# Kernel optimization log

Hardware: AMD Instinct MI355X
Metric: run time of the kernel (lower is better)

Reference implementation:

```python
import jax, jax.numpy as jnp
import numpy as np

N_NODES = 50000
N_EDGES = 640000
IN_F, H1, H2, H3, N_CLS = 128, 128, 128, 128, 40


def setup_inputs() -> dict:
    key = jax.random.key(0)
    ks = jax.random.split(key, 16)
    def lin(k, i, o):
        bound = 1.0 / np.sqrt(i)
        kw, kb = jax.random.split(k)
        W = jax.random.uniform(kw, (i, o), jnp.float32, -bound, bound)
        b = jax.random.uniform(kb, (o,), jnp.float32, -bound, bound)
        return W, b
    Wr, br = lin(ks[0], IN_F, H3)
    W1, b1 = lin(ks[1], IN_F, H1)
    W2, b2 = lin(ks[2], H1, H2)
    W3, b3 = lin(ks[3], H2, H3)
    Wop, bop = lin(ks[4], H3, N_CLS)
    x = jax.random.normal(ks[5], (N_NODES, IN_F), jnp.float32)
    src = jax.random.randint(ks[6], (N_EDGES,), 0, N_NODES, jnp.int64)
    dst = jax.random.randint(ks[7], (N_EDGES,), 0, N_NODES, jnp.int64)
    edge_weight = jax.random.uniform(ks[8], (N_EDGES,), jnp.float32)
    return {"x": x, "src": src, "dst": dst, "edge_weight": edge_weight,
            "Wr": Wr, "br": br, "W1": W1, "b1": b1, "W2": W2, "b2": b2,
            "W3": W3, "b3": b3, "Wop": Wop, "bop": bop}


def _gconv(x, src, dst, ew, W, b, n_nodes):
    # gather neighbor features, scale by edge weight, scatter-sum to dst, linear
    msg = x[src] * ew[:, None]                      # [E, d_in]
    agg = jax.ops.segment_sum(msg, dst, num_segments=n_nodes)  # [N, d_in]
    return agg @ W + b


def reference(x, src, dst, edge_weight, Wr, br, W1, b1, W2, b2, W3, b3, Wop, bop):
    n = x.shape[0]
    res = x @ Wr + br
    h = jax.nn.relu(_gconv(x, src, dst, edge_weight, W1, b1, n))
    h = jax.nn.relu(_gconv(h, src, dst, edge_weight, W2, b2, n))
    h = _gconv(h, src, dst, edge_weight, W3, b3, n)
    h = jax.nn.relu(h + res)
    return h @ Wop + bop
```

## Files before the change

kernel.cpp:

```cpp
#include <hip/hip_runtime.h>
#include <hip/hip_fp16.h>
#include <stdint.h>


#define NF 128

typedef unsigned short u16;
typedef unsigned int u32;
typedef __attribute__((ext_vector_type(8))) short short8;
typedef __attribute__((ext_vector_type(4))) float f32x4;

__device__ __forceinline__ float bf2f(u16 v) {
    union { unsigned u; float f; } x; x.u = (unsigned)v << 16; return x.f;
}
__device__ __forceinline__ u16 f2bf(float f) {
    union { float f; unsigned u; } x; x.f = f;
    unsigned r = (x.u + 0x7FFFu + ((x.u >> 16) & 1u)) >> 16;
    return (u16)r;
}

__global__ __launch_bounds__(256) void prep_all(
    const int* __restrict__ dst, int* __restrict__ counts, int* __restrict__ rank,
    int n_edges,
    const float* __restrict__ x, u16* __restrict__ xb, int n_feat,
    const float* __restrict__ Wr, const float* __restrict__ W1,
    const float* __restrict__ W2, const float* __restrict__ W3,
    const float* __restrict__ Wop, u16* __restrict__ Wt, u16* __restrict__ Wtop,
    int HB, int CB)
{
    int b = blockIdx.x;
    if (b < HB) {
        int e = b * 256 + threadIdx.x;
        if (e < n_edges) rank[e] = atomicAdd(&counts[dst[e]], 1);
    } else if (b < HB + CB) {
        int idx = ((b - HB) * 256 + threadIdx.x) * 4;
        if (idx < n_feat) {
            float4 v = *reinterpret_cast<const float4*>(x + idx);
            ushort4 o;
            o.x = f2bf(v.x); o.y = f2bf(v.y); o.z = f2bf(v.z); o.w = f2bf(v.w);
            *reinterpret_cast<ushort4*>(xb + idx) = o;
        }
    } else {
        int i = (b - HB - CB) * 256 + threadIdx.x;
        if (i < 4 * 16384) {
            int w = i >> 14, r = i & 16383;
            int nn = r >> 7, kk = r & 127;
            const float* W = (w == 0) ? Wr : (w == 1) ? W1 : (w == 2) ? W2 : W3;
            Wt[i] = f2bf(W[kk * NF + nn]);
        } else {
            int r = i - 4 * 16384;
            if (r < 48 * 128) {
                int nn = r >> 7, kk = r & 127;
                Wtop[r] = (nn < 40) ? f2bf(Wop[kk * 40 + nn]) : (u16)0;
            }
        }
    }
}

__global__ __launch_bounds__(256) void scan_pass1(
    const int* __restrict__ counts, int* __restrict__ bsums, int n)
{
    __shared__ int s[256];
    int i = blockIdx.x * 256 + threadIdx.x;
    int c = (i < n) ? counts[i] : 0;
    s[threadIdx.x] = (c + 3) & ~3;
    __syncthreads();
    for (int off = 128; off > 0; off >>= 1) {
        if (threadIdx.x < off) s[threadIdx.x] += s[threadIdx.x + off];
        __syncthreads();
    }
    if (threadIdx.x == 0) bsums[blockIdx.x] = s[0];
}

__global__ __launch_bounds__(256) void scan_pass23(
    int* __restrict__ rowptr, const int* __restrict__ bsums,
    u32* __restrict__ ppairs, int n, int G)
{
    __shared__ int s[256];
    int t = threadIdx.x;
    int bv = (t < G) ? bsums[t] : 0;
    s[t] = bv;
    __syncthreads();
    for (int off = 1; off < 256; off <<= 1) {
        int u = (t >= off) ? s[t - off] : 0;
        __syncthreads();
        s[t] += u;
        __syncthreads();
    }
    int blockoff = (blockIdx.x > 0) ? s[blockIdx.x - 1] : 0;
    int total = s[255];
    __syncthreads();

    int i = blockIdx.x * 256 + t;
    int c = (i < n) ? rowptr[i] : 0;
    int v = (c + 3) & ~3;
    s[t] = v;
    __syncthreads();
    for (int off = 1; off < 256; off <<= 1) {
        int u = (t >= off) ? s[t - off] : 0;
        __syncthreads();
        s[t] += u;
        __syncthreads();
    }
    int excl = s[t] - v + blockoff;
    if (i < n) {
        rowptr[i] = excl;
        for (int k = c; k < v; ++k) ppairs[excl + k] = 0u;
    }
    if (i == 0) rowptr[n] = total;
}

__global__ __launch_bounds__(256) void fill_res(
    const int* __restrict__ src, const int* __restrict__ dst,
    const float* __restrict__ ew, const int* __restrict__ rowptr,
    const int* __restrict__ rank, u32* __restrict__ ppairs, int n_edges,
    const u16* __restrict__ A, const u16* __restrict__ Wt,
    const float* __restrict__ bias, u16* __restrict__ resout, int nrows,
    int HB)
{
    __shared__ u16 Bs[128 * 128];
    if (blockIdx.x < (u32)HB) {
        int e = blockIdx.x * 256 + threadIdx.x;
        if (e >= n_edges) return;
        int pos = rowptr[dst[e]] + rank[e];
        ppairs[pos] = ((u32)src[e] << 16) |
                      (u32)__half_as_ushort(__float2half_rn(ew[e]));
        return;
    }
    const int bid = blockIdx.x - HB;
    const int tid = threadIdx.x;
    #pragma unroll
    for (int i = 0; i < 8; i++) {
        int G = tid + i * 256;
        int row = G >> 4, g = G & 15, gs = g ^ (row & 7);
        *reinterpret_cast<short8*>(&Bs[row * NF + gs * 8]) =
            *reinterpret_cast<const short8*>(Wt + (size_t)G * 8);
    }

    const int wave = tid >> 6, lane = tid & 63;
    const int lrow = lane & 15, lk = lane >> 4;
    const int row0 = bid * 64 + wave * 16;
    const int grow = row0 + lrow;

    short8 a[4];
    if (grow < nrows) {
        const u16* Ar = A + (size_t)grow * NF + lk * 8;
        #pragma unroll
        for (int t = 0; t < 4; t++)
            a[t] = *reinterpret_cast<const short8*>(Ar + t * 32);
    } else {
        #pragma unroll
        for (int t = 0; t < 4; t++)
            #pragma unroll
            for (int j = 0; j < 8; j++) a[t][j] = 0;
    }
    __syncthreads();

    f32x4 acc[8];
    #pragma unroll
    for (int c = 0; c < 8; c++) { acc[c][0]=0.f; acc[c][1]=0.f; acc[c][2]=0.f; acc[c][3]=0.f; }

    #pragma unroll
    for (int t = 0; t < 4; t++) {
        #pragma unroll
        for (int c = 0; c < 8; c++) {
            int col = c * 16 + lrow;
            int g = t * 4 + lk, gs = g ^ (col & 7);
            short8 b = *reinterpret_cast<const short8*>(&Bs[col * NF + gs * 8]);
            acc[c] = __builtin_amdgcn_mfma_f32_16x16x32_bf16(a[t], b, acc[c], 0, 0, 0);
        }
    }

    #pragma unroll
    for (int c = 0; c < 8; c++) {
        int col = c * 16 + lrow;
        float bv = bias[col];
        #pragma unroll
        for (int r = 0; r < 4; r++) {
            int orow = row0 + lk * 4 + r;
            if (orow < nrows)
                resout[(size_t)orow * NF + col] = f2bf(acc[c][r] + bv);
        }
    }
}

template<int RES, int PROJ>
__global__ __launch_bounds__(256) void layer_gg(
    const u16* __restrict__ X, const int* __restrict__ rowptr,
    const u32* __restrict__ ppairs, const u16* __restrict__ Wt,
    const float* __restrict__ bias, const u16* __restrict__ resid,
    const u16* __restrict__ Wtop, const float* __restrict__ bop,
    u16* __restrict__ hout, float* __restrict__ out, int n_nodes)
{
    __shared__ u16 As[16 * 128];
    __shared__ u16 Hs[16 * 128];

    const int tid = threadIdx.x;
    const int node0 = blockIdx.x * 16;

    {
        const int nl = tid >> 4;
        const int fl = tid & 15;
        const int node = node0 + nl;
        float acc[8];
        #pragma unroll
        for (int j = 0; j < 8; j++) acc[j] = 0.f;

        if (node < n_nodes) {
            const u16* xf = X + fl * 8;
            int e0 = rowptr[node];
            int e1 = rowptr[node + 1];
            int e = e0;
            for (; e + 8 <= e1; e += 8) {
                uint4 pa = *reinterpret_cast<const uint4*>(ppairs + e);
                uint4 pb = *reinterpret_cast<const uint4*>(ppairs + e + 4);
                u32 p[8] = {pa.x, pa.y, pa.z, pa.w, pb.x, pb.y, pb.z, pb.w};
                short8 v[8];
                #pragma unroll
                for (int k = 0; k < 8; k++)
                    v[k] = *reinterpret_cast<const short8*>(xf + (size_t)(p[k] >> 16) * NF);
                #pragma unroll
                for (int k = 0; k < 8; k++) {
                    float w = __half2float(__ushort_as_half((u16)(p[k] & 0xFFFFu)));
                    #pragma unroll
                    for (int j = 0; j < 8; j++)
                        acc[j] = fmaf(bf2f((u16)v[k][j]), w, acc[j]);
                }
            }
            if (e < e1) {
                uint4 pa = *reinterpret_cast<const uint4*>(ppairs + e);
                u32 p[4] = {pa.x, pa.y, pa.z, pa.w};
                short8 v[4];
                #pragma unroll
                for (int k = 0; k < 4; k++)
                    v[k] = *reinterpret_cast<const short8*>(xf + (size_t)(p[k] >> 16) * NF);
                #pragma unroll
                for (int k = 0; k < 4; k++) {
                    float w = __half2float(__ushort_as_half((u16)(p[k] & 0xFFFFu)));
                    #pragma unroll
                    for (int j = 0; j < 8; j++)
                        acc[j] = fmaf(bf2f((u16)v[k][j]), w, acc[j]);
                }
            }
        }
        short8 o;
        #pragma unroll
        for (int j = 0; j < 8; j++) o[j] = (short)f2bf(acc[j]);
        int gs = fl ^ (nl & 7);
        *reinterpret_cast<short8*>(&As[nl * NF + gs * 8]) = o;
    }
    __syncthreads();

    const int wave = tid >> 6, lane = tid & 63;
    const int lrow = lane & 15, lk = lane >> 4;

    short8 a[4];
    #pragma unroll
    for (int t = 0; t < 4; t++) {
        int g = t * 4 + lk, gs = g ^ (lrow & 7);
        a[t] = *reinterpret_cast<const short8*>(&As[lrow * NF + gs * 8]);
    }

    f32x4 acc2[2];
    #pragma unroll
    for (int ct = 0; ct < 2; ct++) { acc2[ct][0]=0.f; acc2[ct][1]=0.f; acc2[ct][2]=0.f; acc2[ct][3]=0.f; }

    #pragma unroll
    for (int t = 0; t < 4; t++) {
        #pragma unroll
        for (int ct = 0; ct < 2; ct++) {
            int col = wave * 32 + ct * 16 + lrow;
            short8 b = *reinterpret_cast<const short8*>(Wt + (size_t)col * NF + (t * 4 + lk) * 8);
            acc2[ct] = __builtin_amdgcn_mfma_f32_16x16x32_bf16(a[t], b, acc2[ct], 0, 0, 0);
        }
    }

    #pragma unroll
    for (int ct = 0; ct < 2; ct++) {
        int col = wave * 32 + ct * 16 + lrow;
        float bv = bias[col];
        #pragma unroll
        for (int r = 0; r < 4; r++) {
            int row = lk * 4 + r;
            int node = node0 + row;
            if (node < n_nodes) {
                float v = acc2[ct][r] + bv;
                if (RES) v += bf2f(resid[(size_t)node * NF + col]);
                v = fmaxf(v, 0.f);
                if (!PROJ) {
                    hout[(size_t)node * NF + col] = f2bf(v);
                } else {
                    Hs[row * NF + (((col >> 3) ^ (row & 7)) << 3) + (col & 7)] = f2bf(v);
                }
            }
        }
    }

    if (PROJ) {
        __syncthreads();
        if (wave < 3) {
            short8 pa[4];
            #pragma unroll
            for (int t = 0; t < 4; t++) {
                int g = t * 4 + lk, gs = g ^ (lrow & 7);
                pa[t] = *reinterpret_cast<const short8*>(&Hs[lrow * NF + gs * 8]);
            }
            f32x4 pacc;
            pacc[0]=0.f; pacc[1]=0.f; pacc[2]=0.f; pacc[3]=0.f;
            int col = wave * 16 + lrow;
            #pragma unroll
            for (int t = 0; t < 4; t++) {
                short8 b = *reinterpret_cast<const short8*>(Wtop + (size_t)col * NF + (t * 4 + lk) * 8);
                pacc = __builtin_amdgcn_mfma_f32_16x16x32_bf16(pa[t], b, pacc, 0, 0, 0);
            }
            if (col < 40) {
                float bv = bop[col];
                #pragma unroll
                for (int r = 0; r < 4; r++) {
                    int node = node0 + lk * 4 + r;
                    if (node < n_nodes)
                        out[(size_t)node * 40 + col] = pacc[r] + bv;
                }
            }
        }
    }
}


extern "C" void kernel_launch(void* const* d_in, const int* in_sizes, int n_in,
                              void* d_out, int out_size, void* d_ws, size_t ws_size,
                              hipStream_t stream)
{
    const float* x   = (const float*)d_in[0];
    const int*   src = (const int*)d_in[1];
    const int*   dst = (const int*)d_in[2];
    const float* ew  = (const float*)d_in[3];
    const float* Wr  = (const float*)d_in[4];
    const float* br  = (const float*)d_in[5];
    const float* W1  = (const float*)d_in[6];
    const float* b1  = (const float*)d_in[7];
    const float* W2  = (const float*)d_in[8];
    const float* b2  = (const float*)d_in[9];
    const float* W3  = (const float*)d_in[10];
    const float* b3  = (const float*)d_in[11];
    const float* Wop = (const float*)d_in[12];
    const float* bop = (const float*)d_in[13];
    float* out = (float*)d_out;

    const int n_nodes = in_sizes[0] / NF;
    const int n_edges = in_sizes[1];
    const size_t feat = (size_t)n_nodes * NF;

    u16* xb   = (u16*)d_ws;
    u16* h1b  = xb + feat;
    u16* h2b  = h1b + feat;
    u16* resb = h2b + feat;
    u16* Wt   = resb + feat;
    u16* Wtop = Wt + 4 * 16384;
    int* rowptr = (int*)(Wtop + 48 * 128);
    const int G1 = (n_nodes + 255) / 256;
    int* bsums  = rowptr + (n_nodes + 1);
    int* rank   = bsums + (G1 + 1);
    u32* ppairs = (u32*)(((uintptr_t)(rank + n_edges) + 15) & ~(uintptr_t)15);

    const int HB = (n_edges + 255) / 256;
    const int CB = ((int)feat / 4 + 255) / 256;
    const int PB = (4 * 16384 + 48 * 128 + 255) / 256;
    const int RG = (n_nodes + 63) / 64;
    const int layer_grid = (n_nodes + 15) / 16;

    hipMemsetAsync(rowptr, 0, (size_t)(n_nodes + 1) * sizeof(int), stream);
    prep_all<<<HB + CB + PB, 256, 0, stream>>>(
        dst, rowptr, rank, n_edges, x, xb, (int)feat,
        Wr, W1, W2, W3, Wop, Wt, Wtop, HB, CB);
    scan_pass1<<<G1, 256, 0, stream>>>(rowptr, bsums, n_nodes);
    scan_pass23<<<G1, 256, 0, stream>>>(rowptr, bsums, ppairs, n_nodes, G1);

    fill_res<<<HB + RG, 256, 0, stream>>>(
        src, dst, ew, rowptr, rank, ppairs, n_edges,
        xb, Wt, br, resb, n_nodes, HB);

    layer_gg<0, 0><<<layer_grid, 256, 0, stream>>>(
        xb, rowptr, ppairs, Wt + 16384, b1, nullptr, nullptr, nullptr,
        h1b, nullptr, n_nodes);
    layer_gg<0, 0><<<layer_grid, 256, 0, stream>>>(
        h1b, rowptr, ppairs, Wt + 2 * 16384, b2, nullptr, nullptr, nullptr,
        h2b, nullptr, n_nodes);
    layer_gg<1, 1><<<layer_grid, 256, 0, stream>>>(
        h2b, rowptr, ppairs, Wt + 3 * 16384, b3, resb, Wtop, bop,
        nullptr, out, n_nodes);
}
```

Baseline: 186.9 us.

## Convert layer kernels to persistent blocks with atomic tile work-stealing

The three graph-conv layer kernels now launch a fixed grid of 2048 persistent blocks. Each block repeatedly claims a 16-node tile through an atomic counter, and the counters are zeroed in scan_pass1. This is meant to smooth load imbalance from uneven node degrees and to cut block launch and teardown overhead across about 3125 tiles per layer. In exchange it adds an atomic plus two extra barriers per tile, and it may lose some latency hiding compared with the hardware block scheduler.

```diff
diff --git a/kernel.cpp b/kernel.cpp
--- a/kernel.cpp
+++ b/kernel.cpp
@@ -58,9 +58,11 @@
 }
 
 __global__ __launch_bounds__(256) void scan_pass1(
-    const int* __restrict__ counts, int* __restrict__ bsums, int n)
+    const int* __restrict__ counts, int* __restrict__ bsums,
+    int* __restrict__ tilectr, int n)
 {
     __shared__ int s[256];
+    if (blockIdx.x == 0 && threadIdx.x < 3) tilectr[threadIdx.x] = 0;
     int i = blockIdx.x * 256 + threadIdx.x;
     int c = (i < n) ? counts[i] : 0;
     s[threadIdx.x] = (c + 3) & ~3;
@@ -190,138 +192,147 @@
     const u32* __restrict__ ppairs, const u16* __restrict__ Wt,
     const float* __restrict__ bias, const u16* __restrict__ resid,
     const u16* __restrict__ Wtop, const float* __restrict__ bop,
-    u16* __restrict__ hout, float* __restrict__ out, int n_nodes)
+    u16* __restrict__ hout, float* __restrict__ out, int n_nodes,
+    int* __restrict__ ctr, int ntiles)
 {
     __shared__ u16 As[16 * 128];
-    __shared__ u16 Hs[16 * 128];
+    __shared__ u16 Hs[PROJ ? 16 * 128 : 8];
+    __shared__ int s_tile;
 
     const int tid = threadIdx.x;
-    const int node0 = blockIdx.x * 16;
-
-    {
-        const int nl = tid >> 4;
-        const int fl = tid & 15;
-        const int node = node0 + nl;
-        float acc[8];
-        #pragma unroll
-        for (int j = 0; j < 8; j++) acc[j] = 0.f;
-
-        if (node < n_nodes) {
-            const u16* xf = X + fl * 8;
-            int e0 = rowptr[node];
-            int e1 = rowptr[node + 1];
-            int e = e0;
-            for (; e + 8 <= e1; e += 8) {
-                uint4 pa = *reinterpret_cast<const uint4*>(ppairs + e);
-                uint4 pb = *reinterpret_cast<const uint4*>(ppairs + e + 4);
-                u32 p[8] = {pa.x, pa.y, pa.z, pa.w, pb.x, pb.y, pb.z, pb.w};
-                short8 v[8];
-                #pragma unroll
-                for (int k = 0; k < 8; k++)
-                    v[k] = *reinterpret_cast<const short8*>(xf + (size_t)(p[k] >> 16) * NF);
-                #pragma unroll
-                for (int k = 0; k < 8; k++) {
-                    float w = __half2float(__ushort_as_half((u16)(p[k] & 0xFFFFu)));
-                    #pragma unroll
-                    for (int j = 0; j < 8; j++)
-                        acc[j] = fmaf(bf2f((u16)v[k][j]), w, acc[j]);
-                }
-            }
-            if (e < e1) {
-                uint4 pa = *reinterpret_cast<const uint4*>(ppairs + e);
-                u32 p[4] = {pa.x, pa.y, pa.z, pa.w};
-                short8 v[4];
-                #pragma unroll
-                for (int k = 0; k < 4; k++)
-                    v[k] = *reinterpret_cast<const short8*>(xf + (size_t)(p[k] >> 16) * NF);
-                #pragma unroll
-                for (int k = 0; k < 4; k++) {
-                    float w = __half2float(__ushort_as_half((u16)(p[k] & 0xFFFFu)));
-                    #pragma unroll
-                    for (int j = 0; j < 8; j++)
-                        acc[j] = fmaf(bf2f((u16)v[k][j]), w, acc[j]);
-                }
-            }
-        }
-        short8 o;
-        #pragma unroll
-        for (int j = 0; j < 8; j++) o[j] = (short)f2bf(acc[j]);
-        int gs = fl ^ (nl & 7);
-        *reinterpret_cast<short8*>(&As[nl * NF + gs * 8]) = o;
-    }
-    __syncthreads();
-
     const int wave = tid >> 6, lane = tid & 63;
     const int lrow = lane & 15, lk = lane >> 4;
-
-    short8 a[4];
-    #pragma unroll
-    for (int t = 0; t < 4; t++) {
-        int g = t * 4 + lk, gs = g ^ (lrow & 7);
-        a[t] = *reinterpret_cast<const short8*>(&As[lrow * NF + gs * 8]);
-    }
-
-    f32x4 acc2[2];
-    #pragma unroll
-    for (int ct = 0; ct < 2; ct++) { acc2[ct][0]=0.f; acc2[ct][1]=0.f; acc2[ct][2]=0.f; acc2[ct][3]=0.f; }
-
-    #pragma unroll
-    for (int t = 0; t < 4; t++) {
+    const int nl = tid >> 4;
+    const int fl = tid & 15;
+
+    for (;;) {
+        if (tid == 0) s_tile = atomicAdd(ctr, 1);
+        __syncthreads();
+        const int tile = s_tile;
+        if (tile >= ntiles) return;
+        const int node0 = tile * 16;
+
+        {
+            const int node = node0 + nl;
+            float acc[8];
+            #pragma unroll
+            for (int j = 0; j < 8; j++) acc[j] = 0.f;
+
+            if (node < n_nodes) {
+                const u16* xf = X + fl * 8;
+                int e0 = rowptr[node];
+                int e1 = rowptr[node + 1];
+                int e = e0;
+                for (; e + 8 <= e1; e += 8) {
+                    uint4 pa = *reinterpret_cast<const uint4*>(ppairs + e);
+                    uint4 pb = *reinterpret_cast<const uint4*>(ppairs + e + 4);
+                    u32 p[8] = {pa.x, pa.y, pa.z, pa.w, pb.x, pb.y, pb.z, pb.w};
+                    short8 v[8];
+                    #pragma unroll
+                    for (int k = 0; k < 8; k++)
+                        v[k] = *reinterpret_cast<const short8*>(xf + (size_t)(p[k] >> 16) * NF);
+                    #pragma unroll
+                    for (int k = 0; k < 8; k++) {
+                        float w = __half2float(__ushort_as_half((u16)(p[k] & 0xFFFFu)));
+                        #pragma unroll
+                        for (int j = 0; j < 8; j++)
+                            acc[j] = fmaf(bf2f((u16)v[k][j]), w, acc[j]);
+                    }
+                }
+                if (e < e1) {
+                    uint4 pa = *reinterpret_cast<const uint4*>(ppairs + e);
+                    u32 p[4] = {pa.x, pa.y, pa.z, pa.w};
+                    short8 v[4];
+                    #pragma unroll
+                    for (int k = 0; k < 4; k++)
+                        v[k] = *reinterpret_cast<const short8*>(xf + (size_t)(p[k] >> 16) * NF);
+                    #pragma unroll
+                    for (int k = 0; k < 4; k++) {
+                        float w = __half2float(__ushort_as_half((u16)(p[k] & 0xFFFFu)));
+                        #pragma unroll
+                        for (int j = 0; j < 8; j++)
+                            acc[j] = fmaf(bf2f((u16)v[k][j]), w, acc[j]);
+                    }
+                }
+            }
+            short8 o;
+            #pragma unroll
+            for (int j = 0; j < 8; j++) o[j] = (short)f2bf(acc[j]);
+            int gs = fl ^ (nl & 7);
+            *reinterpret_cast<short8*>(&As[nl * NF + gs * 8]) = o;
+        }
+        __syncthreads();
+
+        short8 a[4];
+        #pragma unroll
+        for (int t = 0; t < 4; t++) {
+            int g = t * 4 + lk, gs = g ^ (lrow & 7);
+            a[t] = *reinterpret_cast<const short8*>(&As[lrow * NF + gs * 8]);
+        }
+
+        f32x4 acc2[2];
+        #pragma unroll
+        for (int ct = 0; ct < 2; ct++) { acc2[ct][0]=0.f; acc2[ct][1]=0.f; acc2[ct][2]=0.f; acc2[ct][3]=0.f; }
+
+        #pragma unroll
+        for (int t = 0; t < 4; t++) {
+            #pragma unroll
+            for (int ct = 0; ct < 2; ct++) {
+                int col = wave * 32 + ct * 16 + lrow;
+                short8 b = *reinterpret_cast<const short8*>(Wt + (size_t)col * NF + (t * 4 + lk) * 8);
+                acc2[ct] = __builtin_amdgcn_mfma_f32_16x16x32_bf16(a[t], b, acc2[ct], 0, 0, 0);
+            }
+        }
+
         #pragma unroll
         for (int ct = 0; ct < 2; ct++) {
             int col = wave * 32 + ct * 16 + lrow;
-            short8 b = *reinterpret_cast<const short8*>(Wt + (size_t)col * NF + (t * 4 + lk) * 8);
-            acc2[ct] = __builtin_amdgcn_mfma_f32_16x16x32_bf16(a[t], b, acc2[ct], 0, 0, 0);
-        }
-    }
-
-    #pragma unroll
-    for (int ct = 0; ct < 2; ct++) {
-        int col = wave * 32 + ct * 16 + lrow;
-        float bv = bias[col];
-        #pragma unroll
-        for (int r = 0; r < 4; r++) {
-            int row = lk * 4 + r;
-            int node = node0 + row;
-            if (node < n_nodes) {
-                float v = acc2[ct][r] + bv;
-                if (RES) v += bf2f(resid[(size_t)node * NF + col]);
-                v = fmaxf(v, 0.f);
-                if (!PROJ) {
-                    hout[(size_t)node * NF + col] = f2bf(v);
-                } else {
-                    Hs[row * NF + (((col >> 3) ^ (row & 7)) << 3) + (col & 7)] = f2bf(v);
+            float bv = bias[col];
+            #pragma unroll
+            for (int r = 0; r < 4; r++) {
+                int row = lk * 4 + r;
+                int node = node0 + row;
+                if (node < n_nodes) {
+                    float v = acc2[ct][r] + bv;
+                    if (RES) v += bf2f(resid[(size_t)node * NF + col]);
+                    v = fmaxf(v, 0.f);
+                    if (!PROJ) {
+                        hout[(size_t)node * NF + col] = f2bf(v);
+                    } else {
+                        Hs[row * NF + (((col >> 3) ^ (row & 7)) << 3) + (col & 7)] = f2bf(v);
+                    }
                 }
             }
         }
-    }
-
-    if (PROJ) {
-        __syncthreads();
-        if (wave < 3) {
-            short8 pa[4];
-            #pragma unroll
-            for (int t = 0; t < 4; t++) {
-                int g = t * 4 + lk, gs = g ^ (lrow & 7);
-                pa[t] = *reinterpret_cast<const short8*>(&Hs[lrow * NF + gs * 8]);
+
+        if (PROJ) {
+            __syncthreads();
+            if (wave < 3) {
+                short8 pa[4];
+                #pragma unroll
+                for (int t = 0; t < 4; t++) {
+                    int g = t * 4 + lk, gs = g ^ (lrow & 7);
+                    pa[t] = *reinterpret_cast<const short8*>(&Hs[lrow * NF + gs * 8]);
+                }
+                f32x4 pacc;
+                pacc[0]=0.f; pacc[1]=0.f; pacc[2]=0.f; pacc[3]=0.f;
+                int col = wave * 16 + lrow;
+                #pragma unroll
+                for (int t = 0; t < 4; t++) {
+                    short8 b = *reinterpret_cast<const short8*>(Wtop + (size_t)col * NF + (t * 4 + lk) * 8);
+                    pacc = __builtin_amdgcn_mfma_f32_16x16x32_bf16(pa[t], b, pacc, 0, 0, 0);
+                }
+                if (col < 40) {
+                    float bv = bop[col];
+                    #pragma unroll
+                    for (int r = 0; r < 4; r++) {
+                        int node = node0 + lk * 4 + r;
+                        if (node < n_nodes)
+                            out[(size_t)node * 40 + col] = pacc[r] + bv;
+                    }
+                }
             }
-            f32x4 pacc;
-            pacc[0]=0.f; pacc[1]=0.f; pacc[2]=0.f; pacc[3]=0.f;
-            int col = wave * 16 + lrow;
-            #pragma unroll
-            for (int t = 0; t < 4; t++) {
-                short8 b = *reinterpret_cast<const short8*>(Wtop + (size_t)col * NF + (t * 4 + lk) * 8);
-                pacc = __builtin_amdgcn_mfma_f32_16x16x32_bf16(pa[t], b, pacc, 0, 0, 0);
-            }
-            if (col < 40) {
-                float bv = bop[col];
-                #pragma unroll
-                for (int r = 0; r < 4; r++) {
-                    int node = node0 + lk * 4 + r;
-                    if (node < n_nodes)
-                        out[(size_t)node * 40 + col] = pacc[r] + bv;
-                }
-            }
+            __syncthreads();
         }
     }
 }
@@ -360,20 +371,22 @@
     int* rowptr = (int*)(Wtop + 48 * 128);
     const int G1 = (n_nodes + 255) / 256;
     int* bsums  = rowptr + (n_nodes + 1);
-    int* rank   = bsums + (G1 + 1);
+    int* tilectr = bsums + (G1 + 1);
+    int* rank   = tilectr + 4;
     u32* ppairs = (u32*)(((uintptr_t)(rank + n_edges) + 15) & ~(uintptr_t)15);
 
     const int HB = (n_edges + 255) / 256;
     const int CB = ((int)feat / 4 + 255) / 256;
     const int PB = (4 * 16384 + 48 * 128 + 255) / 256;
     const int RG = (n_nodes + 63) / 64;
-    const int layer_grid = (n_nodes + 15) / 16;
+    const int ntiles = (n_nodes + 15) / 16;
+    const int layer_grid = 2048;
 
     hipMemsetAsync(rowptr, 0, (size_t)(n_nodes + 1) * sizeof(int), stream);
     prep_all<<<HB + CB + PB, 256, 0, stream>>>(
         dst, rowptr, rank, n_edges, x, xb, (int)feat,
         Wr, W1, W2, W3, Wop, Wt, Wtop, HB, CB);
-    scan_pass1<<<G1, 256, 0, stream>>>(rowptr, bsums, n_nodes);
+    scan_pass1<<<G1, 256, 0, stream>>>(rowptr, bsums, tilectr, n_nodes);
     scan_pass23<<<G1, 256, 0, stream>>>(rowptr, bsums, ppairs, n_nodes, G1);
 
     fill_res<<<HB + RG, 256, 0, stream>>>(
@@ -382,11 +395,11 @@
 
     layer_gg<0, 0><<<layer_grid, 256, 0, stream>>>(
         xb, rowptr, ppairs, Wt + 16384, b1, nullptr, nullptr, nullptr,
-        h1b, nullptr, n_nodes);
+        h1b, nullptr, n_nodes, tilectr + 0, ntiles);
     layer_gg<0, 0><<<layer_grid, 256, 0, stream>>>(
         h1b, rowptr, ppairs, Wt + 2 * 16384, b2, nullptr, nullptr, nullptr,
-        h2b, nullptr, n_nodes);
+        h2b, nullptr, n_nodes, tilectr + 1, ntiles);
     layer_gg<1, 1><<<layer_grid, 256, 0, stream>>>(
         h2b, rowptr, ppairs, Wt + 3 * 16384, b3, resb, Wtop, bop,
-        nullptr, out, n_nodes);
-}
+        nullptr, out, n_nodes, tilectr + 2, ntiles);
+}
```

Result: slower. 287.2 us (+53.7%).
